# Kernel tuning notes

Hardware: AMD Instinct MI355X
Metric: run time of the kernel (lower is better)

Reference implementation:

```python
import jax, jax.numpy as jnp
import numpy as np
from jax import lax

B, J, H, W = 64, 17, 96, 96
TOPK = 8


def setup_inputs() -> dict:
    key = jax.random.key(0)
    k1, k2, k3, k4 = jax.random.split(key, 4)
    output_s = jax.random.normal(k1, (B, J, H, W), dtype=jnp.float32)
    output_t = jax.random.normal(k2, (B, J, H, W), dtype=jnp.float32)
    target = jax.random.uniform(k3, (B, J, H, W), dtype=jnp.float32)
    # make half the joints have max(gt) == 1 exactly, to exercise both branches
    target = target.at[:, : J // 2, 0, 0].set(1.0)
    target_weight = jax.random.uniform(k4, (B, J, 1), dtype=jnp.float32)
    return {
        "output_s": output_s,
        "output_t": output_t,
        "target": target,
        "target_weight": target_weight,
        "effective_num_joints": 17,
    }


def reference(output_s, output_t, target, target_weight, effective_num_joints):
    b, j = output_t.shape[0], output_t.shape[1]
    s = output_s.reshape(b, j, -1)  # [B, J, HW]
    t = output_t.reshape(b, j, -1)
    g = target.reshape(b, j, -1)
    w = target_weight  # [B, J, 1] broadcasts over HW

    # per-joint condition: max over batch+pixels of (unweighted) gt == 1
    cond = (jnp.max(g, axis=(0, 2)) == 1.0)  # [J]

    sw, tw, gw = s * w, t * w, g * w
    d_sg = (sw - gw) ** 2  # [B, J, HW]
    d_st = (sw - tw) ** 2

    # elementwise per-joint loss, then mean over pixels -> [B, J]
    per = 0.5 * jnp.where(cond[None, :, None], d_sg, d_sg + d_st)
    loss_mat = per.mean(axis=2)  # [B, J]

    # OHKM: per-sample top-k over joints, averaged
    topk_vals, _ = lax.top_k(loss_mat, TOPK)  # [B, k]
    ohkm_loss_s = jnp.mean(jnp.sum(topk_vals, axis=1) / TOPK)

    # accumulated mean-MSE over joints
    m_sg = d_sg.mean(axis=(0, 2))  # [J]
    m_st = d_st.mean(axis=(0, 2))
    mse_loss_s = jnp.sum(jnp.where(cond, m_sg, m_sg + m_st))

    final_loss = ohkm_loss_s + mse_loss_s
    return (ohkm_loss_s, mse_loss_s / effective_num_joints, final_loss)
```

## Files before the change

kernel.cpp:

```cpp
#include <hip/hip_runtime.h>
#include <math.h>

#define NB 64
#define NJ 17
#define HW 9216
#define NBJ (NB * NJ)
#define TOPK_K 8
#define NSEG 3
#define SEG_F4 (HW / 4 / NSEG)
#define BLK 256
#define F4_PER_THR (SEG_F4 / BLK)
#define P2T 512

__global__ __launch_bounds__(BLK) void pass1_kernel(
    const float* __restrict__ s,
    const float* __restrict__ t,
    const float* __restrict__ g,
    float* __restrict__ ws)
{
    const int bj  = blockIdx.x / NSEG;
    const int seg = blockIdx.x % NSEG;
    const size_t base4 = (size_t)bj * (HW / 4) + (size_t)seg * SEG_F4;
    const float4* __restrict__ s4 = (const float4*)s + base4;
    const float4* __restrict__ t4 = (const float4*)t + base4;
    const float4* __restrict__ g4 = (const float4*)g + base4;

    float4 a[F4_PER_THR], b[F4_PER_THR], c[F4_PER_THR];
    #pragma unroll
    for (int k = 0; k < F4_PER_THR; ++k) a[k] = s4[threadIdx.x + k * BLK];
    #pragma unroll
    for (int k = 0; k < F4_PER_THR; ++k) b[k] = t4[threadIdx.x + k * BLK];
    #pragma unroll
    for (int k = 0; k < F4_PER_THR; ++k) c[k] = g4[threadIdx.x + k * BLK];

    float ssg = 0.f, sst = 0.f, mg = -INFINITY;

    #define ACCUM(av, bv, cv)                                \
        {                                                    \
            float d1 = (av) - (cv), d2 = (av) - (bv);        \
            ssg += d1 * d1; sst += d2 * d2;                  \
            mg = fmaxf(mg, (cv));                            \
        }

    #pragma unroll
    for (int k = 0; k < F4_PER_THR; ++k) {
        ACCUM(a[k].x, b[k].x, c[k].x)
        ACCUM(a[k].y, b[k].y, c[k].y)
        ACCUM(a[k].z, b[k].z, c[k].z)
        ACCUM(a[k].w, b[k].w, c[k].w)
    }
    #undef ACCUM

    #pragma unroll
    for (int off = 32; off > 0; off >>= 1) {
        ssg += __shfl_down(ssg, off);
        sst += __shfl_down(sst, off);
        mg = fmaxf(mg, __shfl_down(mg, off));
    }

    __shared__ float sh_sg[4], sh_st[4], sh_mg[4];
    const int wave = threadIdx.x >> 6;
    const int lane = threadIdx.x & 63;
    if (lane == 0) { sh_sg[wave] = ssg; sh_st[wave] = sst; sh_mg[wave] = mg; }
    __syncthreads();
    if (threadIdx.x == 0) {
        const float fsg = (sh_sg[0] + sh_sg[1]) + (sh_sg[2] + sh_sg[3]);
        const float fst = (sh_st[0] + sh_st[1]) + (sh_st[2] + sh_st[3]);
        const float fmg = fmaxf(fmaxf(sh_mg[0], sh_mg[1]),
                                fmaxf(sh_mg[2], sh_mg[3]));
        ws[(0 * NSEG + seg) * NBJ + bj] = fsg;
        ws[(1 * NSEG + seg) * NBJ + bj] = fst;
        ws[(2 * NSEG + seg) * NBJ + bj] = fmg;
    }
}

__global__ __launch_bounds__(P2T) void pass2_kernel(
    const float* __restrict__ ws,
    const float* __restrict__ w,
    const int* __restrict__ enj_p,
    float* __restrict__ out)
{
    __shared__ float sh_ssg[NBJ];
    __shared__ float sh_sst[NBJ];
    __shared__ float sh_mg[NBJ];
    __shared__ float cond_sh[NJ];
    __shared__ float msum_sh[NJ];

    const int tid = threadIdx.x;

    for (int i = tid; i < NBJ; i += P2T) {
        float ssg = 0.f, sst = 0.f, mg = -INFINITY;
        #pragma unroll
        for (int seg = 0; seg < NSEG; ++seg) {
            ssg += ws[(0 * NSEG + seg) * NBJ + i];
            sst += ws[(1 * NSEG + seg) * NBJ + i];
            mg = fmaxf(mg, ws[(2 * NSEG + seg) * NBJ + i]);
        }
        const float wv = w[i];
        const float w2 = wv * wv;
        sh_ssg[i] = ssg * w2;
        sh_sst[i] = sst * w2;
        sh_mg[i] = mg;
    }
    __syncthreads();

    if (tid < NJ * 16) {
        const int j = tid >> 4;
        const int sub = tid & 15;
        float ssg = 0.f, sst = 0.f, mg = -INFINITY;
        for (int bb = sub; bb < NB; bb += 16) {
            ssg += sh_ssg[bb * NJ + j];
            sst += sh_sst[bb * NJ + j];
            mg = fmaxf(mg, sh_mg[bb * NJ + j]);
        }
        #pragma unroll
        for (int off = 8; off > 0; off >>= 1) {
            ssg += __shfl_down(ssg, off);
            sst += __shfl_down(sst, off);
            mg = fmaxf(mg, __shfl_down(mg, off));
        }
        if (sub == 0) {
            const bool cond = (mg == 1.0f);
            cond_sh[j] = cond ? 1.f : 0.f;
            const float inv_bhw = 1.f / (float)(NB * HW);
            msum_sh[j] = cond ? (ssg * inv_bhw) : ((ssg + sst) * inv_bhw);
        }
    }
    __syncthreads();

    if (tid < NB) {
        float lm[NJ];
        const float inv_hw = 1.f / (float)HW;
        #pragma unroll
        for (int j = 0; j < NJ; ++j) {
            const float ssg = sh_ssg[tid * NJ + j];
            const float sst = sh_sst[tid * NJ + j];
            const float v = (cond_sh[j] != 0.f) ? ssg : (ssg + sst);
            lm[j] = 0.5f * v * inv_hw;
        }
        float tk = 0.f;
        for (int k = 0; k < TOPK_K; ++k) {
            int mi = 0;
            float mv = lm[0];
            #pragma unroll
            for (int j = 1; j < NJ; ++j) {
                if (lm[j] > mv) { mv = lm[j]; mi = j; }
            }
            tk += mv;
            #pragma unroll
            for (int j = 0; j < NJ; ++j) {
                if (j == mi) lm[j] = -INFINITY;
            }
        }
        #pragma unroll
        for (int off = 32; off > 0; off >>= 1) tk += __shfl_down(tk, off);

        if (tid == 0) {
            const float ohkm = tk / (float)(TOPK_K * NB);
            float mse = 0.f;
            for (int j = 0; j < NJ; ++j) mse += msum_sh[j];
            const float enj = (float)(*enj_p);
            out[0] = ohkm;
            out[1] = mse / enj;
            out[2] = ohkm + mse;
        }
    }
}

extern "C" void kernel_launch(void* const* d_in, const int* in_sizes, int n_in,
                              void* d_out, int out_size, void* d_ws, size_t ws_size,
                              hipStream_t stream) {
    const float* output_s = (const float*)d_in[0];
    const float* output_t = (const float*)d_in[1];
    const float* target   = (const float*)d_in[2];
    const float* tweight  = (const float*)d_in[3];
    const int*   enj      = (const int*)d_in[4];
    float* out = (float*)d_out;
    float* ws  = (float*)d_ws;

    pass1_kernel<<<NBJ * NSEG, BLK, 0, stream>>>(output_s, output_t, target, ws);
    pass2_kernel<<<1, P2T, 0, stream>>>(ws, tweight, enj, out);
}
```

Baseline: 145.2 us.

## Fuse finalize pass into main kernel via last-block atomic counter

Merges the two kernels into one: each block writes its partials, then increments a global atomic counter, and the last block to finish performs the cross-block reduction, top-k and final outputs. This removes the second kernel launch and its dependency gap, but adds a memset of the counter before launch plus a threadfence and atomic per block. The finalize now runs in a single 256-thread block instead of 512 threads, so that tail step has less parallelism.

```diff
diff --git a/kernel.cpp b/kernel.cpp
--- a/kernel.cpp
+++ b/kernel.cpp
@@ -10,14 +10,21 @@
 #define SEG_F4 (HW / 4 / NSEG)
 #define BLK 256
 #define F4_PER_THR (SEG_F4 / BLK)
-#define P2T 512
+#define NBLOCKS (NBJ * NSEG)
+#define WS_OFF 4
 
-__global__ __launch_bounds__(BLK) void pass1_kernel(
+__global__ __launch_bounds__(BLK) void fused_kernel(
     const float* __restrict__ s,
     const float* __restrict__ t,
     const float* __restrict__ g,
-    float* __restrict__ ws)
+    const float* __restrict__ w,
+    const int* __restrict__ enj_p,
+    float* __restrict__ out,
+    float* __restrict__ ws_raw)
 {
+    unsigned int* cnt = (unsigned int*)ws_raw;
+    float* ws = ws_raw + WS_OFF;
+
     const int bj  = blockIdx.x / NSEG;
     const int seg = blockIdx.x % NSEG;
     const size_t base4 = (size_t)bj * (HW / 4) + (size_t)seg * SEG_F4;
@@ -58,72 +65,74 @@
         mg = fmaxf(mg, __shfl_down(mg, off));
     }
 
-    __shared__ float sh_sg[4], sh_st[4], sh_mg[4];
+    __shared__ float sh_sg[4], sh_st[4], sh_mg4[4];
     const int wave = threadIdx.x >> 6;
     const int lane = threadIdx.x & 63;
-    if (lane == 0) { sh_sg[wave] = ssg; sh_st[wave] = sst; sh_mg[wave] = mg; }
+    if (lane == 0) { sh_sg[wave] = ssg; sh_st[wave] = sst; sh_mg4[wave] = mg; }
     __syncthreads();
     if (threadIdx.x == 0) {
         const float fsg = (sh_sg[0] + sh_sg[1]) + (sh_sg[2] + sh_sg[3]);
         const float fst = (sh_st[0] + sh_st[1]) + (sh_st[2] + sh_st[3]);
-        const float fmg = fmaxf(fmaxf(sh_mg[0], sh_mg[1]),
-                                fmaxf(sh_mg[2], sh_mg[3]));
+        const float fmg = fmaxf(fmaxf(sh_mg4[0], sh_mg4[1]),
+                                fmaxf(sh_mg4[2], sh_mg4[3]));
         ws[(0 * NSEG + seg) * NBJ + bj] = fsg;
         ws[(1 * NSEG + seg) * NBJ + bj] = fst;
         ws[(2 * NSEG + seg) * NBJ + bj] = fmg;
     }
-}
 
-__global__ __launch_bounds__(P2T) void pass2_kernel(
-    const float* __restrict__ ws,
-    const float* __restrict__ w,
-    const int* __restrict__ enj_p,
-    float* __restrict__ out)
-{
+    __shared__ int is_last;
+    if (threadIdx.x == 0) {
+        __threadfence();
+        const unsigned old = atomicAdd(cnt, 1u);
+        is_last = (old == (unsigned)(NBLOCKS - 1)) ? 1 : 0;
+    }
+    __syncthreads();
+    if (!is_last) return;
+    __threadfence();
+
     __shared__ float sh_ssg[NBJ];
     __shared__ float sh_sst[NBJ];
-    __shared__ float sh_mg[NBJ];
+    __shared__ float sh_mgA[NBJ];
     __shared__ float cond_sh[NJ];
     __shared__ float msum_sh[NJ];
-
     const int tid = threadIdx.x;
 
-    for (int i = tid; i < NBJ; i += P2T) {
-        float ssg = 0.f, sst = 0.f, mg = -INFINITY;
+    for (int i = tid; i < NBJ; i += BLK) {
+        float fsg = 0.f, fst = 0.f, fmg = -INFINITY;
         #pragma unroll
-        for (int seg = 0; seg < NSEG; ++seg) {
-            ssg += ws[(0 * NSEG + seg) * NBJ + i];
-            sst += ws[(1 * NSEG + seg) * NBJ + i];
-            mg = fmaxf(mg, ws[(2 * NSEG + seg) * NBJ + i]);
+        for (int sg2 = 0; sg2 < NSEG; ++sg2) {
+            fsg += ws[(0 * NSEG + sg2) * NBJ + i];
+            fst += ws[(1 * NSEG + sg2) * NBJ + i];
+            fmg = fmaxf(fmg, ws[(2 * NSEG + sg2) * NBJ + i]);
         }
         const float wv = w[i];
         const float w2 = wv * wv;
-        sh_ssg[i] = ssg * w2;
-        sh_sst[i] = sst * w2;
-        sh_mg[i] = mg;
+        sh_ssg[i] = fsg * w2;
+        sh_sst[i] = fst * w2;
+        sh_mgA[i] = fmg;
     }
     __syncthreads();
 
-    if (tid < NJ * 16) {
-        const int j = tid >> 4;
-        const int sub = tid & 15;
-        float ssg = 0.f, sst = 0.f, mg = -INFINITY;
-        for (int bb = sub; bb < NB; bb += 16) {
-            ssg += sh_ssg[bb * NJ + j];
-            sst += sh_sst[bb * NJ + j];
-            mg = fmaxf(mg, sh_mg[bb * NJ + j]);
+    if (tid < NJ * 8) {
+        const int j = tid >> 3;
+        const int sub = tid & 7;
+        float fsg = 0.f, fst = 0.f, fmg = -INFINITY;
+        for (int bb = sub; bb < NB; bb += 8) {
+            fsg += sh_ssg[bb * NJ + j];
+            fst += sh_sst[bb * NJ + j];
+            fmg = fmaxf(fmg, sh_mgA[bb * NJ + j]);
         }
         #pragma unroll
-        for (int off = 8; off > 0; off >>= 1) {
-            ssg += __shfl_down(ssg, off);
-            sst += __shfl_down(sst, off);
-            mg = fmaxf(mg, __shfl_down(mg, off));
+        for (int off = 4; off > 0; off >>= 1) {
+            fsg += __shfl_down(fsg, off);
+            fst += __shfl_down(fst, off);
+            fmg = fmaxf(fmg, __shfl_down(fmg, off));
         }
         if (sub == 0) {
-            const bool cond = (mg == 1.0f);
+            const bool cond = (fmg == 1.0f);
             cond_sh[j] = cond ? 1.f : 0.f;
             const float inv_bhw = 1.f / (float)(NB * HW);
-            msum_sh[j] = cond ? (ssg * inv_bhw) : ((ssg + sst) * inv_bhw);
+            msum_sh[j] = cond ? (fsg * inv_bhw) : ((fsg + fst) * inv_bhw);
         }
     }
     __syncthreads();
@@ -133,9 +142,9 @@
         const float inv_hw = 1.f / (float)HW;
         #pragma unroll
         for (int j = 0; j < NJ; ++j) {
-            const float ssg = sh_ssg[tid * NJ + j];
-            const float sst = sh_sst[tid * NJ + j];
-            const float v = (cond_sh[j] != 0.f) ? ssg : (ssg + sst);
+            const float fsg = sh_ssg[tid * NJ + j];
+            const float fst = sh_sst[tid * NJ + j];
+            const float v = (cond_sh[j] != 0.f) ? fsg : (fsg + fst);
             lm[j] = 0.5f * v * inv_hw;
         }
         float tk = 0.f;
@@ -178,6 +187,7 @@
     float* out = (float*)d_out;
     float* ws  = (float*)d_ws;
 
-    pass1_kernel<<<NBJ * NSEG, BLK, 0, stream>>>(output_s, output_t, target, ws);
-    pass2_kernel<<<1, P2T, 0, stream>>>(ws, tweight, enj, out);
+    hipMemsetAsync(d_ws, 0, 4, stream);
+    fused_kernel<<<NBLOCKS, BLK, 0, stream>>>(output_s, output_t, target,
+                                              tweight, enj, out, ws);
 }
```

After: 299.1 us. +106.0%, slower.
